# Optimization experiments

Hardware: AMD Instinct MI355X
Metric: run time of the kernel (lower is better)

Reference implementation:

```python
import jax, jax.numpy as jnp
import numpy as np
import math

B, S, D_IN, EMBED, H = 4, 1024, 1024, 1024, 16
HD = EMBED // H  # 64


def setup_inputs() -> dict:
    key = jax.random.key(0)
    ks = jax.random.split(key, 8)
    x = jax.random.normal(ks[0], (B, S, D_IN), dtype=jnp.float32)
    mask = jax.random.randint(ks[1], (B, S, S), 0, 2, dtype=jnp.int32)
    weights = jax.random.uniform(ks[2], (B, S, S), dtype=jnp.float32)
    # xavier-uniform-ish scale for projections
    lim_qkv = math.sqrt(6.0 / (D_IN + 3 * EMBED))
    lim_o = math.sqrt(6.0 / (EMBED + EMBED))
    W_qkv = jax.random.uniform(ks[3], (3 * EMBED, D_IN), minval=-lim_qkv, maxval=lim_qkv, dtype=jnp.float32)
    b_qkv = jnp.zeros((3 * EMBED,), dtype=jnp.float32)
    W_o = jax.random.uniform(ks[4], (EMBED, EMBED), minval=-lim_o, maxval=lim_o, dtype=jnp.float32)
    b_o = jnp.zeros((EMBED,), dtype=jnp.float32)
    return {"x": x, "mask": mask, "weights": weights, "W_qkv": W_qkv, "b_qkv": b_qkv, "W_o": W_o, "b_o": b_o}


def reference(x, mask, weights, W_qkv, b_qkv, W_o, b_o):
    b, s, _ = x.shape
    # QKV projection: [b, s, 3*EMBED] -> [b, H, s, 3*HD]
    qkv = (x @ W_qkv.T + b_qkv).reshape(b, s, H, 3 * HD).transpose(0, 2, 1, 3)
    q, k, v = jnp.split(qkv, 3, axis=-1)  # each [b, H, s, HD]
    logits = jnp.einsum('bhqd,bhkd->bhqk', q, k) / math.sqrt(HD)
    logits = jnp.where(mask[:, None, :, :] == 0, jnp.float32(-9e15), logits)
    # weights transposed on last two dims, broadcast over heads
    w = jnp.swapaxes(weights, -2, -1)[:, None, :, :]  # [b, 1, s, s]
    m = jnp.max(logits, axis=-1, keepdims=True)
    e = w * jnp.exp(logits - m)
    attn = e / jnp.sum(e, axis=-1, keepdims=True)
    vals = jnp.einsum('bhqk,bhkd->bhqd', attn, v)
    vals = vals.transpose(0, 2, 1, 3).reshape(b, s, EMBED)
    return vals @ W_o.T + b_o
```

## Files before the change

kernel.cpp:

```cpp
#include <hip/hip_runtime.h>
#include <hip/hip_bf16.h>
#include <stdint.h>

#define SDIM 1024
#define BATCH 4
#define NH 16
#define HDIM 64
#define KDIM 1024
#define N_QKV 3072
#define EMB 1024

typedef uint16_t u16;
typedef __attribute__((ext_vector_type(4))) float f32x4;
typedef __attribute__((ext_vector_type(8))) short bf16x8;
typedef __attribute__((ext_vector_type(8))) unsigned short u16x8;

__device__ __forceinline__ u16 f2bf(float f) {
  union { float f; uint32_t u; } x; x.f = f;
  uint32_t r = x.u + 0x7FFFu + ((x.u >> 16) & 1u);
  return (u16)(r >> 16);
}

__device__ __forceinline__ float bf2f(u16 b) {
  union { uint32_t u; float f; } x; x.u = ((uint32_t)b) << 16;
  return x.f;
}

__device__ __forceinline__ void gload_lds16(const u16* g, u16* l) {
  __builtin_amdgcn_global_load_lds(
      (const __attribute__((address_space(1))) unsigned int*)g,
      (__attribute__((address_space(3))) unsigned int*)l, 16, 0, 0);
}

#define N8_X  524288
#define N8_WQ 393216
#define N8_WO 131072
__global__ void cvt3_kernel(const float* __restrict__ a, const float* __restrict__ b,
                            const float* __restrict__ c,
                            u16* __restrict__ oa, u16* __restrict__ ob, u16* __restrict__ oc) {
  const int total = N8_X + N8_WQ + N8_WO;
  int stride = gridDim.x * blockDim.x;
  for (int i = blockIdx.x * blockDim.x + threadIdx.x; i < total; i += stride) {
    const float* s; u16* d; int j;
    if (i < N8_X)            { s = a; d = oa; j = i; }
    else if (i < N8_X + N8_WQ){ s = b; d = ob; j = i - N8_X; }
    else                     { s = c; d = oc; j = i - N8_X - N8_WQ; }
    const float4* s4 = (const float4*)s + (size_t)j * 2;
    float4 u = s4[0], v = s4[1];
    u16x8 o;
    o[0] = f2bf(u.x); o[1] = f2bf(u.y); o[2] = f2bf(u.z); o[3] = f2bf(u.w);
    o[4] = f2bf(v.x); o[5] = f2bf(v.y); o[6] = f2bf(v.z); o[7] = f2bf(v.w);
    ((u16x8*)d)[j] = o;
  }
}

__global__ __launch_bounds__(512, 2) void gemm_qkv_wm3(
    const u16* __restrict__ A, const u16* __restrict__ Bm,
    const float* __restrict__ bias,
    u16* __restrict__ Qh, u16* __restrict__ Kh, u16* __restrict__ Vt,
    const int* __restrict__ mask, const float* __restrict__ wts, u16* __restrict__ wm3)
{
  __shared__ char smem[131072];
  const int tid = threadIdx.x;

  if (blockIdx.x < 192) {
    const int gid = blockIdx.x;
    const int brow = (gid & 15) * 256, bcol = (gid >> 4) * 256;
    const int wid = tid >> 6, lane = tid & 63;
    const int g = lane >> 4, c = lane & 15, cx = c & 7;
    const int wr = wid >> 2, wc = wid & 3;

    const u16* asrc[4]; const u16* bsrc[4]; int doff[4];
    #pragma unroll
    for (int j = 0; j < 4; ++j) {
      int i = j * 512 + tid;
      int row = i >> 3, sch = (i & 7) ^ (row & 7);
      asrc[j] = A  + (size_t)(brow + row) * KDIM + sch * 8;
      bsrc[j] = Bm + (size_t)(bcol + row) * KDIM + sch * 8;
      doff[j] = (j * 512 + wid * 64) * 16;
    }

    auto stage = [&](int kt, int slot) {
      char* base = smem + slot * 65536;
      #pragma unroll
      for (int j = 0; j < 4; ++j)
        gload_lds16(asrc[j] + kt * 64, (u16*)(base + doff[j]));
      #pragma unroll
      for (int j = 0; j < 4; ++j)
        gload_lds16(bsrc[j] + kt * 64, (u16*)(base + 32768 + doff[j]));
    };

    f32x4 acc[8][4] = {};

    stage(0, 0);
    __syncthreads();

    for (int kt = 0; kt < 16; ++kt) {
      if (kt < 15) stage(kt + 1, (kt + 1) & 1);

      const char* As = smem + (kt & 1) * 65536;
      const char* Bs = As + 32768;

      #pragma unroll
      for (int kk = 0; kk < 2; ++kk) {
        bf16x8 af[8], bfr[4];
        #pragma unroll
        for (int m = 0; m < 8; ++m) {
          int row = wr * 128 + m * 16 + c;
          af[m] = *(const bf16x8*)(As + (row << 7) + ((((kk << 2) + g) ^ cx) << 4));
        }
        #pragma unroll
        for (int n = 0; n < 4; ++n) {
          int row = wc * 64 + n * 16 + c;
          bfr[n] = *(const bf16x8*)(Bs + (row << 7) + ((((kk << 2) + g) ^ cx) << 4));
        }
        __builtin_amdgcn_s_setprio(1);
        #pragma unroll
        for (int m = 0; m < 8; ++m)
          #pragma unroll
          for (int n = 0; n < 4; ++n)
            acc[m][n] = __builtin_amdgcn_mfma_f32_16x16x32_bf16(
                af[m], bfr[n], acc[m][n], 0, 0, 0);
        __builtin_amdgcn_s_setprio(0);
      }
      __syncthreads();
    }

    #pragma unroll
    for (int m = 0; m < 8; ++m) {
      #pragma unroll
      for (int n = 0; n < 4; ++n) {
        int col = bcol + wc * 64 + n * 16 + c;
        float bv = bias[col];
        int h = col / 192;
        int rem = col - h * 192;
        int sec = rem >> 6, d = rem & 63;
        #pragma unroll
        for (int r = 0; r < 4; ++r) {
          int row = brow + wr * 128 + m * 16 + g * 4 + r;
          int b = row >> 10, sl = row & 1023;
          float v = acc[m][n][r] + bv;
          if (sec == 0)
            Qh[((size_t)(b * NH + h) * SDIM + sl) * HDIM + d] = f2bf(v * 0.125f);
          else if (sec == 1)
            Kh[((size_t)(b * NH + h) * SDIM + sl) * HDIM + d] = f2bf(v);
          else
            Vt[((size_t)(b * NH + h) * HDIM + d) * SDIM + sl] = f2bf(v);
        }
      }
    }
  } else {
    const int wmid = blockIdx.x - 192;
    const size_t SS = (size_t)SDIM * SDIM;
    int   (*mt)[68] = (int(*)[68])smem;
    float (*wt)[68] = (float(*)[68])(smem + 17408);

    #pragma unroll
    for (int tt = 0; tt < 2; ++tt) {
      const int id = wmid * 2 + tt;
      const int kt = id & 15, qt = (id >> 4) & 15, b = id >> 8;
      const int q0 = qt * 64, k0 = kt * 64;
      if (tt) __syncthreads();

      #pragma unroll
      for (int j = 0; j < 2; ++j) {
        int idx = j * 512 + tid;
        int row = idx >> 4, c4 = idx & 15;
        int4 m4 = *(const int4*)(mask + (size_t)b * SS + (size_t)(q0 + row) * SDIM + k0 + c4 * 4);
        mt[row][c4 * 4 + 0] = m4.x; mt[row][c4 * 4 + 1] = m4.y;
        mt[row][c4 * 4 + 2] = m4.z; mt[row][c4 * 4 + 3] = m4.w;
        float4 w4 = *(const float4*)(wts + (size_t)b * SS + (size_t)(k0 + row) * SDIM + q0 + c4 * 4);
        wt[row][c4 * 4 + 0] = w4.x; wt[row][c4 * 4 + 1] = w4.y;
        wt[row][c4 * 4 + 2] = w4.z; wt[row][c4 * 4 + 3] = w4.w;
      }
      __syncthreads();

      const int st2 = tid >> 6, lane = tid & 63, g2 = lane >> 4, c2 = lane & 15;
      const int st = st2 & 3, wh = st2 >> 2;
      const int kl = st * 16 + c2;
      #pragma unroll
      for (int wq = 0; wq < 2; ++wq) {
        int wid2 = wh * 2 + wq;
        ushort4 o;
        u16* oe = (u16*)&o;
        #pragma unroll
        for (int r = 0; r < 4; ++r) {
          int ql = wid2 * 16 + g2 * 4 + r;
          oe[r] = mt[ql][kl] ? f2bf(wt[kl][ql]) : (u16)0;
        }
        size_t off = (((((size_t)b * 16 + qt) * 4 + wid2) * 16 + kt) * 4 + st) * 256 + (g2 * 16 + c2) * 4;
        *(ushort4*)(wm3 + off) = o;
      }
    }
  }
}

__global__ __launch_bounds__(256) void gemm_bt(
    const u16* __restrict__ A, const u16* __restrict__ Bm,
    const float* __restrict__ bias, float* __restrict__ C,
    int M, int N, int K)
{
  __shared__ u16 As[128 * 64];
  __shared__ u16 Bs[128 * 64];
  const int tid = threadIdx.x;
  const int wid = tid >> 6, lane = tid & 63;
  const int g = lane >> 4, c = lane & 15, cx = c & 7;
  const int wrow = (wid >> 1) * 64, wcol = (wid & 1) * 64;
  const int brow = blockIdx.x * 128, bcol = blockIdx.y * 128;

  const u16* asrc[4]; const u16* bsrc[4]; u16* adst[4]; u16* bdst[4];
  #pragma unroll
  for (int j = 0; j < 4; ++j) {
    int ci = j * 256 + tid;
    int row = ci >> 3, sch = (ci & 7) ^ (row & 7);
    asrc[j] = A  + (size_t)(brow + row) * K + sch * 8;
    bsrc[j] = Bm + (size_t)(bcol + row) * K + sch * 8;
    adst[j] = As + (j * 256 + wid * 64) * 8;
    bdst[j] = Bs + (j * 256 + wid * 64) * 8;
  }

  f32x4 acc[4][4] = {};
  const char* Asc = (const char*)As;
  const char* Bsc = (const char*)Bs;

  for (int kt = 0; kt < K / 64; ++kt) {
    #pragma unroll
    for (int j = 0; j < 4; ++j) {
      gload_lds16(asrc[j] + kt * 64, adst[j]);
      gload_lds16(bsrc[j] + kt * 64, bdst[j]);
    }
    __syncthreads();

    bf16x8 af[2][4], bfr[2][4];
    #pragma unroll
    for (int kk = 0; kk < 2; ++kk)
      #pragma unroll
      for (int i = 0; i < 4; ++i) {
        int cha = ((kk << 2) + g) ^ cx;
        af[kk][i]  = *(const bf16x8*)(Asc + ((wrow + i * 16 + c) << 7) + (cha << 4));
        bfr[kk][i] = *(const bf16x8*)(Bsc + ((wcol + i * 16 + c) << 7) + (cha << 4));
      }
    #pragma unroll
    for (int kk = 0; kk < 2; ++kk)
      #pragma unroll
      for (int mi = 0; mi < 4; ++mi)
        #pragma unroll
        for (int ni = 0; ni < 4; ++ni)
          acc[mi][ni] = __builtin_amdgcn_mfma_f32_16x16x32_bf16(
              af[kk][mi], bfr[kk][ni], acc[mi][ni], 0, 0, 0);
    __syncthreads();
  }

  #pragma unroll
  for (int mi = 0; mi < 4; ++mi)
    #pragma unroll
    for (int ni = 0; ni < 4; ++ni) {
      int col = bcol + wcol + ni * 16 + c;
      float bv = bias[col];
      #pragma unroll
      for (int r = 0; r < 4; ++r) {
        int row = brow + wrow + mi * 16 + g * 4 + r;
        C[(size_t)row * N + col] = acc[mi][ni][r] + bv;
      }
    }
}

__global__ __launch_bounds__(256, 3) void attn_kernel(
    const u16* __restrict__ Qh, const u16* __restrict__ Kh, const u16* __restrict__ Vt,
    const u16* __restrict__ wm3, u16* __restrict__ vals)
{
  int bid = blockIdx.x;
  int swz = (bid & 7) * 128 + (bid >> 3);
  const int qt = swz & 15, bh = swz >> 4;
  const int h = bh & 15, b = bh >> 4;

  const int tid = threadIdx.x;
  const int wid = tid >> 6, lane = tid & 63;
  const int g = lane >> 4, c = lane & 15;
  const int qloc = qt * 64 + wid * 16;

  __shared__ u16 Kb[2][4096];
  __shared__ u16 Vb[2][4096];
  __shared__ u16 Plds[4][16 * 72];
  char* pw = (char*)&Plds[wid][0];

  const u16* qp = Qh + ((size_t)bh * SDIM + qloc + c) * HDIM;
  bf16x8 qa0 = *(const bf16x8*)(qp + g * 8);
  bf16x8 qa1 = *(const bf16x8*)(qp + 32 + g * 8);

  const u16* kbase = Kh + (size_t)bh * SDIM * HDIM;
  const u16* vbase = Vt + (size_t)bh * HDIM * SDIM;
  const u16* wbase = wm3 + ((((size_t)(b * 16 + qt) * 4 + wid) * 16) * 4) * 256 + (g * 16 + c) * 4;

  float l_run[4] = {0.f, 0.f, 0.f, 0.f};
  f32x4 acc_o[4] = {};
  const int xr = (c & 8) << 2;
  const int cx = c & 7;

  auto stage = [&](int buf, int kt) {
    const int k0 = kt * 64;
    #pragma unroll
    for (int j = 0; j < 2; ++j) {
      int i = j * 256 + tid;
      int row = i >> 3, sch = (i & 7) ^ (row & 7);
      gload_lds16(kbase + (size_t)(k0 + row) * HDIM + sch * 8,
                  &Kb[buf][(size_t)(j * 256 + wid * 64) * 8]);
      gload_lds16(vbase + (size_t)row * SDIM + k0 + sch * 8,
                  &Vb[buf][(size_t)(j * 256 + wid * 64) * 8]);
    }
  };

  stage(0, 0);
  __syncthreads();
  int cur = 0;

  for (int kt = 0; kt < 16; ++kt) {
    if (kt < 15) stage(cur ^ 1, kt + 1);

    ushort4 w4[4];
    #pragma unroll
    for (int st = 0; st < 4; ++st)
      w4[st] = *(const ushort4*)(wbase + (size_t)(kt * 4 + st) * 256);

    const char* kb = (const char*)&Kb[cur][0];
    const char* vb = (const char*)&Vb[cur][0];

    f32x4 sc[4];
    #pragma unroll
    for (int st = 0; st < 4; ++st) {
      int ro = (st * 16 + c) * 128;
      bf16x8 kb0 = *(const bf16x8*)(kb + ro + ((g ^ cx) << 4));
      bf16x8 kb1 = *(const bf16x8*)(kb + ro + (((4 + g) ^ cx) << 4));
      f32x4 z = {};
      z = __builtin_amdgcn_mfma_f32_16x16x32_bf16(qa0, kb0, z, 0, 0, 0);
      z = __builtin_amdgcn_mfma_f32_16x16x32_bf16(qa1, kb1, z, 0, 0, 0);
      sc[st] = z;
    }

    bf16x8 vb0[4], vb1[4];
    #pragma unroll
    for (int dt = 0; dt < 4; ++dt) {
      int ro = (dt * 16 + c) * 128;
      vb0[dt] = *(const bf16x8*)(vb + ro + ((g ^ cx) << 4));
      vb1[dt] = *(const bf16x8*)(vb + ro + (((4 + g) ^ cx) << 4));
    }

    #pragma unroll
    for (int st = 0; st < 4; ++st) {
      #pragma unroll
      for (int r = 0; r < 4; ++r) {
        float w = bf2f(((const u16*)&w4[st])[r]);
        float p = w * __expf(sc[st][r]);
        u16 pb = f2bf(p);
        l_run[r] += bf2f(pb);
        int row = g * 4 + r;
        int colb = (st * 16 + c) * 2;
        *(u16*)(pw + row * 144 + (colb ^ ((row & 8) << 2))) = pb;
      }
    }

    bf16x8 pa0 = *(const bf16x8*)(pw + c * 144 + ((g * 16) ^ xr));
    bf16x8 pa1 = *(const bf16x8*)(pw + c * 144 + ((64 + g * 16) ^ xr));

    #pragma unroll
    for (int dt = 0; dt < 4; ++dt) {
      acc_o[dt] = __builtin_amdgcn_mfma_f32_16x16x32_bf16(pa0, vb0[dt], acc_o[dt], 0, 0, 0);
      acc_o[dt] = __builtin_amdgcn_mfma_f32_16x16x32_bf16(pa1, vb1[dt], acc_o[dt], 0, 0, 0);
    }

    __syncthreads();
    cur ^= 1;
  }

  #pragma unroll
  for (int r = 0; r < 4; ++r) {
    #pragma unroll
    for (int o = 1; o < 16; o <<= 1) l_run[r] += __shfl_xor(l_run[r], o);
  }
  float inv[4];
  #pragma unroll
  for (int r = 0; r < 4; ++r) inv[r] = 1.0f / l_run[r];

  #pragma unroll
  for (int dt = 0; dt < 4; ++dt)
    #pragma unroll
    for (int r = 0; r < 4; ++r) {
      int row = b * SDIM + qloc + g * 4 + r;
      vals[(size_t)row * EMB + h * HDIM + dt * 16 + c] = f2bf(acc_o[dt][r] * inv[r]);
    }
}

extern "C" void kernel_launch(void* const* d_in, const int* in_sizes, int n_in,
                              void* d_out, int out_size, void* d_ws, size_t ws_size,
                              hipStream_t stream) {
  const float* x     = (const float*)d_in[0];
  const int*   mask  = (const int*)d_in[1];
  const float* wts   = (const float*)d_in[2];
  const float* W_qkv = (const float*)d_in[3];
  const float* b_qkv = (const float*)d_in[4];
  const float* W_o   = (const float*)d_in[5];
  const float* b_o   = (const float*)d_in[6];
  float* out = (float*)d_out;

  char* ws = (char*)d_ws;
  u16* xb   = (u16*)(ws);
  u16* wqb  = (u16*)(ws + (8ull  << 20));
  u16* wob  = (u16*)(ws + (14ull << 20));
  u16* Qh   = (u16*)(ws + (16ull << 20));
  u16* Kh   = (u16*)(ws + (24ull << 20));
  u16* Vt   = (u16*)(ws + (32ull << 20));
  u16* valb = (u16*)(ws + (40ull << 20));
  u16* wm3b = (u16*)d_out;

  cvt3_kernel<<<2048, 256, 0, stream>>>(x, W_qkv, W_o, xb, wqb, wob);

  gemm_qkv_wm3<<<704, 512, 0, stream>>>(xb, wqb, b_qkv, Qh, Kh, Vt, mask, wts, wm3b);

  attn_kernel<<<1024, 256, 0, stream>>>(Qh, Kh, Vt, wm3b, valb);

  dim3 g3(32, 8);
  gemm_bt<<<g3, 256, 0, stream>>>(valb, wob, b_o, out, BATCH * SDIM, EMB, KDIM);
}
```

Before: 125.5 us.

## Compute transposed scores so P feeds PV MFMA from registers, dropping LDS round-trip

Swaps the QK^T MFMA operand order so each lane holds a row of P laid out exactly as the A operand of the PV MFMA. P is packed to bf16 with v_cvt_pk_bf16_f32 and used directly, which removes the per-wave LDS scratch buffer and its writes and reads. K rows are read in a permuted order with a new XOR swizzle to match, and the mask/weight preprocessing is rewritten to emit the matching 16-byte-per-lane layout. The row-sum reduction shrinks to two cross-group shuffles, and launch bounds are raised to 4 blocks per SM for more occupancy, which may add register pressure.

```diff
diff --git a/kernel.cpp b/kernel.cpp
--- a/kernel.cpp
+++ b/kernel.cpp
@@ -152,8 +152,8 @@
   } else {
     const int wmid = blockIdx.x - 192;
     const size_t SS = (size_t)SDIM * SDIM;
-    int   (*mt)[68] = (int(*)[68])smem;
-    float (*wt)[68] = (float(*)[68])(smem + 17408);
+    int   (*mt)[69] = (int(*)[69])smem;
+    float (*wt)[69] = (float(*)[69])(smem + 17664);
 
     #pragma unroll
     for (int tt = 0; tt < 2; ++tt) {
@@ -175,22 +175,17 @@
       }
       __syncthreads();
 
-      const int st2 = tid >> 6, lane = tid & 63, g2 = lane >> 4, c2 = lane & 15;
-      const int st = st2 & 3, wh = st2 >> 2;
-      const int kl = st * 16 + c2;
-      #pragma unroll
-      for (int wq = 0; wq < 2; ++wq) {
-        int wid2 = wh * 2 + wq;
-        ushort4 o;
-        u16* oe = (u16*)&o;
-        #pragma unroll
-        for (int r = 0; r < 4; ++r) {
-          int ql = wid2 * 16 + g2 * 4 + r;
-          oe[r] = mt[ql][kl] ? f2bf(wt[kl][ql]) : (u16)0;
-        }
-        size_t off = (((((size_t)b * 16 + qt) * 4 + wid2) * 16 + kt) * 4 + st) * 256 + (g2 * 16 + c2) * 4;
-        *(ushort4*)(wm3 + off) = o;
-      }
+      const int wid2 = tid >> 7, hf = (tid >> 6) & 1, lane = tid & 63;
+      const int g2 = lane >> 4, c2 = lane & 15;
+      const int ql = wid2 * 16 + c2;
+      u16x8 o;
+      #pragma unroll
+      for (int e = 0; e < 8; ++e) {
+        int kl = 8 * g2 + 4 * (e >> 2) + (e & 3) + 32 * hf;
+        o[e] = mt[ql][kl] ? f2bf(wt[kl][ql]) : (u16)0;
+      }
+      size_t off = ((((size_t)(b * 16 + qt) * 4 + wid2) * 16 + kt)) * 1024 + lane * 16 + hf * 8;
+      *(u16x8*)(wm3 + off) = o;
     }
   }
 }
@@ -265,7 +260,7 @@
     }
 }
 
-__global__ __launch_bounds__(256, 3) void attn_kernel(
+__global__ __launch_bounds__(256, 4) void attn_kernel(
     const u16* __restrict__ Qh, const u16* __restrict__ Kh, const u16* __restrict__ Vt,
     const u16* __restrict__ wm3, u16* __restrict__ vals)
 {
@@ -281,8 +276,6 @@
 
   __shared__ u16 Kb[2][4096];
   __shared__ u16 Vb[2][4096];
-  __shared__ u16 Plds[4][16 * 72];
-  char* pw = (char*)&Plds[wid][0];
 
   const u16* qp = Qh + ((size_t)bh * SDIM + qloc + c) * HDIM;
   bf16x8 qa0 = *(const bf16x8*)(qp + g * 8);
@@ -290,19 +283,34 @@
 
   const u16* kbase = Kh + (size_t)bh * SDIM * HDIM;
   const u16* vbase = Vt + (size_t)bh * HDIM * SDIM;
-  const u16* wbase = wm3 + ((((size_t)(b * 16 + qt) * 4 + wid) * 16) * 4) * 256 + (g * 16 + c) * 4;
-
-  float l_run[4] = {0.f, 0.f, 0.f, 0.f};
+  const u16* wbase = wm3 + (((size_t)(b * 16 + qt) * 4 + wid) * 16) * 1024 + lane * 16;
+
+  float l_run = 0.f;
   f32x4 acc_o[4] = {};
-  const int xr = (c & 8) << 2;
-  const int cx = c & 7;
+
+  auto fsw = [](int row) { return ((row ^ (row >> 3)) & 7) ^ ((row & 1) << 2); };
+
+  int kro[4], kxr[4], vro[4], vxr[4];
+  #pragma unroll
+  for (int st = 0; st < 4; ++st) {
+    int kr = ((c >> 2) << 3) + ((st & 1) << 2) + (c & 3) + ((st >> 1) << 5);
+    kro[st] = kr << 7;
+    kxr[st] = fsw(kr);
+  }
+  #pragma unroll
+  for (int dt = 0; dt < 4; ++dt) {
+    int vr = dt * 16 + c;
+    vro[dt] = vr << 7;
+    vxr[dt] = fsw(vr);
+  }
 
   auto stage = [&](int buf, int kt) {
     const int k0 = kt * 64;
     #pragma unroll
     for (int j = 0; j < 2; ++j) {
       int i = j * 256 + tid;
-      int row = i >> 3, sch = (i & 7) ^ (row & 7);
+      int row = i >> 3;
+      int sch = (i & 7) ^ (((row ^ (row >> 3)) & 7) ^ ((row & 1) << 2));
       gload_lds16(kbase + (size_t)(k0 + row) * HDIM + sch * 8,
                   &Kb[buf][(size_t)(j * 256 + wid * 64) * 8]);
       gload_lds16(vbase + (size_t)row * SDIM + k0 + sch * 8,
@@ -317,10 +325,8 @@
   for (int kt = 0; kt < 16; ++kt) {
     if (kt < 15) stage(cur ^ 1, kt + 1);
 
-    ushort4 w4[4];
-    #pragma unroll
-    for (int st = 0; st < 4; ++st)
-      w4[st] = *(const ushort4*)(wbase + (size_t)(kt * 4 + st) * 256);
+    u16x8 w0 = *(const u16x8*)(wbase + kt * 1024);
+    u16x8 w1 = *(const u16x8*)(wbase + kt * 1024 + 8);
 
     const char* kb = (const char*)&Kb[cur][0];
     const char* vb = (const char*)&Vb[cur][0];
@@ -328,58 +334,56 @@
     f32x4 sc[4];
     #pragma unroll
     for (int st = 0; st < 4; ++st) {
-      int ro = (st * 16 + c) * 128;
-      bf16x8 kb0 = *(const bf16x8*)(kb + ro + ((g ^ cx) << 4));
-      bf16x8 kb1 = *(const bf16x8*)(kb + ro + (((4 + g) ^ cx) << 4));
+      bf16x8 ka0 = *(const bf16x8*)(kb + kro[st] + ((g ^ kxr[st]) << 4));
+      bf16x8 ka1 = *(const bf16x8*)(kb + kro[st] + (((4 + g) ^ kxr[st]) << 4));
       f32x4 z = {};
-      z = __builtin_amdgcn_mfma_f32_16x16x32_bf16(qa0, kb0, z, 0, 0, 0);
-      z = __builtin_amdgcn_mfma_f32_16x16x32_bf16(qa1, kb1, z, 0, 0, 0);
+      z = __builtin_amdgcn_mfma_f32_16x16x32_bf16(ka0, qa0, z, 0, 0, 0);
+      z = __builtin_amdgcn_mfma_f32_16x16x32_bf16(ka1, qa1, z, 0, 0, 0);
       sc[st] = z;
     }
 
-    bf16x8 vb0[4], vb1[4];
+    float p[4][4];
+    #pragma unroll
+    for (int st = 0; st < 4; ++st) {
+      #pragma unroll
+      for (int r = 0; r < 4; ++r) {
+        u16 wv = (st < 2) ? ((const u16*)&w0)[st * 4 + r]
+                          : ((const u16*)&w1)[(st - 2) * 4 + r];
+        float pv = bf2f(wv) * __expf(sc[st][r]);
+        p[st][r] = pv;
+        l_run += pv;
+      }
+    }
+
+    uint32_t pk[8];
+    #pragma unroll
+    for (int i = 0; i < 8; ++i) {
+      float lo = p[i >> 1][(i & 1) * 2], hi = p[i >> 1][(i & 1) * 2 + 1];
+      asm("v_cvt_pk_bf16_f32 %0, %1, %2" : "=v"(pk[i]) : "v"(lo), "v"(hi));
+    }
+    union PA { uint32_t u[4]; bf16x8 v; } a0, a1;
+    #pragma unroll
+    for (int i = 0; i < 4; ++i) { a0.u[i] = pk[i]; a1.u[i] = pk[4 + i]; }
+
     #pragma unroll
     for (int dt = 0; dt < 4; ++dt) {
-      int ro = (dt * 16 + c) * 128;
-      vb0[dt] = *(const bf16x8*)(vb + ro + ((g ^ cx) << 4));
-      vb1[dt] = *(const bf16x8*)(vb + ro + (((4 + g) ^ cx) << 4));
-    }
-
-    #pragma unroll
-    for (int st = 0; st < 4; ++st) {
-      #pragma unroll
-      for (int r = 0; r < 4; ++r) {
-        float w = bf2f(((const u16*)&w4[st])[r]);
-        float p = w * __expf(sc[st][r]);
-        u16 pb = f2bf(p);
-        l_run[r] += bf2f(pb);
-        int row = g * 4 + r;
-        int colb = (st * 16 + c) * 2;
-        *(u16*)(pw + row * 144 + (colb ^ ((row & 8) << 2))) = pb;
-      }
-    }
-
-    bf16x8 pa0 = *(const bf16x8*)(pw + c * 144 + ((g * 16) ^ xr));
-    bf16x8 pa1 = *(const bf16x8*)(pw + c * 144 + ((64 + g * 16) ^ xr));
-
-    #pragma unroll
-    for (int dt = 0; dt < 4; ++dt) {
-      acc_o[dt] = __builtin_amdgcn_mfma_f32_16x16x32_bf16(pa0, vb0[dt], acc_o[dt], 0, 0, 0);
-      acc_o[dt] = __builtin_amdgcn_mfma_f32_16x16x32_bf16(pa1, vb1[dt], acc_o[dt], 0, 0, 0);
+      bf16x8 vb0 = *(const bf16x8*)(vb + vro[dt] + ((g ^ vxr[dt]) << 4));
+      bf16x8 vb1 = *(const bf16x8*)(vb + vro[dt] + (((4 + g) ^ vxr[dt]) << 4));
+      acc_o[dt] = __builtin_amdgcn_mfma_f32_16x16x32_bf16(a0.v, vb0, acc_o[dt], 0, 0, 0);
+      acc_o[dt] = __builtin_amdgcn_mfma_f32_16x16x32_bf16(a1.v, vb1, acc_o[dt], 0, 0, 0);
     }
 
     __syncthreads();
     cur ^= 1;
   }
 
-  #pragma unroll
-  for (int r = 0; r < 4; ++r) {
-    #pragma unroll
-    for (int o = 1; o < 16; o <<= 1) l_run[r] += __shfl_xor(l_run[r], o);
-  }
+  l_run += __shfl_xor(l_run, 16);
+  l_run += __shfl_xor(l_run, 32);
+
   float inv[4];
   #pragma unroll
-  for (int r = 0; r < 4; ++r) inv[r] = 1.0f / l_run[r];
+  for (int r = 0; r < 4; ++r)
+    inv[r] = 1.0f / __shfl(l_run, g * 4 + r);
 
   #pragma unroll
   for (int dt = 0; dt < 4; ++dt)
```

After: 108.5 us. 13.5% less time.
